# Kernel optimization log

Measured on AMD Instinct MI355X. Metric: run time of the kernel, lower is better.

Reference implementation:

```python
import jax, jax.numpy as jnp
import numpy as np

NUM_CAPSULE = 16
DIM_CAPSULE = 32
ROUTINGS = 4
EPS = 1e-07


def squash(x, axis=-1):
    # NOTE: faithful to the source: x / sqrt(sum(x^2) + eps) (unit-norm style),
    # NOT the standard Hinton squash.
    s2 = jnp.sum(x * x, axis=axis, keepdims=True)
    return x / jnp.sqrt(s2 + EPS)


def setup_inputs() -> dict:
    key = jax.random.key(0)
    k1, k2 = jax.random.split(key)
    B, N_in, D_in = 128, 1024, 256
    x = jax.random.normal(k1, (B, N_in, D_in), dtype=jnp.float32)
    # xavier_normal over (1, D_in, NUM_CAPSULE*DIM_CAPSULE)
    fan_in, fan_out = D_in, NUM_CAPSULE * DIM_CAPSULE
    std = np.sqrt(2.0 / (fan_in + fan_out))
    W = jax.random.normal(k2, (1, D_in, NUM_CAPSULE * DIM_CAPSULE), dtype=jnp.float32) * std
    return {"x": x, "W": W}


def reference(x, W):
    B, N_in, _ = x.shape
    # u_hat: [B, N_in, num_cap*dim_cap] -> [B, num_cap, N_in, dim_cap]
    u_hat = jnp.matmul(x, W[0])
    u_hat = u_hat.reshape(B, N_in, NUM_CAPSULE, DIM_CAPSULE).transpose(0, 2, 1, 3)

    b = jnp.zeros((B, NUM_CAPSULE, N_in), dtype=u_hat.dtype)
    outputs = None
    for i in range(ROUTINGS):
        # torch permutes to softmax over the num_capsule axis; equivalent to axis=1 here
        c = jax.nn.softmax(b, axis=1)                      # [B, num_cap, N_in]
        outputs = squash(jnp.einsum('bij,bijk->bik', c, u_hat))  # [B, num_cap, dim_cap]
        if i < ROUTINGS - 1:
            b = jnp.einsum('bik,bijk->bij', outputs, u_hat)
    return outputs
```

## Files before the change

### kernel.cpp

```cpp
#include <hip/hip_runtime.h>
#include <hip/hip_bf16.h>

typedef unsigned int u32;
typedef float f32x4 __attribute__((ext_vector_type(4)));
typedef __bf16 bf16x8 __attribute__((ext_vector_type(8)));

#define BATCH 128
#define NIN   1024
#define DIN   256
#define NC    16
#define DC    32
#define NCOL  512

__device__ __forceinline__ float bflo(u32 v){ return __uint_as_float(v << 16); }
__device__ __forceinline__ float bfhi(u32 v){ return __uint_as_float(v & 0xffff0000u); }
__device__ __forceinline__ u32 bfround(u32 ua){ return (ua + 0x7fffu + ((ua >> 16) & 1u)) >> 16; }
__device__ __forceinline__ u32 pack2(float a, float b){
    return (bfround(__float_as_uint(a)) & 0xffffu) | (bfround(__float_as_uint(b)) << 16);
}
__device__ __forceinline__ bf16x8 ldfrag(const u32* p){
    return __builtin_bit_cast(bf16x8, *(const uint4*)p);
}

__global__ __launch_bounds__(256) void k_wconv(const float* __restrict__ W, uint4* __restrict__ Wt2){
    int id = blockIdx.x * 256 + threadIdx.x;
    int l = id & 63, ks = (id >> 6) & 7, ntile = id >> 9;
    int n = ntile * 16 + (l & 15);
    int w0 = ks * 16 + (l >> 4) * 4;
    u32 r[4];
    #pragma unroll
    for (int e = 0; e < 4; e++){
        int w = w0 + e;
        r[e] = pack2(W[(size_t)(2 * w) * NCOL + n], W[(size_t)(2 * w + 1) * NCOL + n]);
    }
    Wt2[id] = make_uint4(r[0], r[1], r[2], r[3]);
}

__global__ __launch_bounds__(512) void k_gemm(const float* __restrict__ x, const uint4* __restrict__ Wt2,
                                              u32* __restrict__ uhat, float* __restrict__ y0){
    __shared__ __align__(16) u32 xl[64 * 128];
    const int t = threadIdx.x, jb = blockIdx.x, b = blockIdx.y;
    const int lane = t & 63, wv = t >> 6;
    const int l15 = lane & 15, q = lane >> 4;

    {
        const float4* xg = (const float4*)(x + ((size_t)b * NIN + jb * 64) * DIN);
        #pragma unroll
        for (int m = 0; m < 4; m++){
            int p = t + 512 * m;
            float4 a = xg[2 * p], c = xg[2 * p + 1];
            int j = p >> 5, wq = 4 * (p & 31);
            uint4 v;
            v.x = pack2(a.x, a.y); v.y = pack2(a.z, a.w);
            v.z = pack2(c.x, c.y); v.w = pack2(c.z, c.w);
            *(uint4*)&xl[j * 128 + ((wq + 4 * j) & 127)] = v;
        }
    }
    __syncthreads();

    f32x4 acc[4][4];
    #pragma unroll
    for (int mt = 0; mt < 4; mt++)
        #pragma unroll
        for (int nt = 0; nt < 4; nt++) acc[mt][nt] = (f32x4){0.f, 0.f, 0.f, 0.f};
    #pragma unroll
    for (int ks = 0; ks < 8; ks++){
        bf16x8 af[4], bfr[4];
        #pragma unroll
        for (int mt = 0; mt < 4; mt++){
            int jr = mt * 16 + l15;
            af[mt] = ldfrag(&xl[jr * 128 + ((ks * 16 + q * 4 + 4 * jr) & 127)]);
        }
        #pragma unroll
        for (int nt = 0; nt < 4; nt++)
            bfr[nt] = __builtin_bit_cast(bf16x8, Wt2[(size_t)(((wv * 4 + nt) * 8 + ks) * 64) + lane]);
        #pragma unroll
        for (int mt = 0; mt < 4; mt++)
            #pragma unroll
            for (int nt = 0; nt < 4; nt++)
                acc[mt][nt] = __builtin_amdgcn_mfma_f32_16x16x32_bf16(af[mt], bfr[nt], acc[mt][nt], 0, 0, 0);
    }

    #pragma unroll
    for (int nt = 0; nt < 4; nt++){
        float v = 0.f;
        #pragma unroll
        for (int mt = 0; mt < 4; mt++)
            #pragma unroll
            for (int r = 0; r < 4; r++) v += acc[mt][nt][r];
        v += __shfl_xor(v, 16);
        v += __shfl_xor(v, 32);
        if (lane < 16) atomicAdd(&y0[b * NCOL + wv * 64 + nt * 16 + lane], v);
    }

    u32* ub = uhat + (((size_t)b * NC + jb) * NCOL) * 32;
    #pragma unroll
    for (int nt = 0; nt < 4; nt++){
        int n = wv * 64 + nt * 16 + l15;
        #pragma unroll
        for (int mt = 0; mt < 4; mt++){
            uint2 v;
            v.x = pack2(acc[mt][nt][0], acc[mt][nt][1]);
            v.y = pack2(acc[mt][nt][2], acc[mt][nt][3]);
            *(uint2*)&ub[n * 32 + mt * 8 + q * 2] = v;
        }
    }
}

__device__ __forceinline__ int rot8(int n){ return (n + (n >> 3)) & 7; }

__global__ __launch_bounds__(256) void k_route_u(const u32* __restrict__ uhat, const float* __restrict__ o,
                                                 float* __restrict__ y){
    __shared__ __align__(16) u32 ul[NCOL * 32];
    __shared__ float ol[NCOL];
    __shared__ float bbc[NC * 68];
    const int jc = blockIdx.x, b = blockIdx.y, t = threadIdx.x;

    ol[t] = o[b * NCOL + t];
    ol[t + 256] = o[b * NCOL + t + 256];
    {
        const uint4* ug = (const uint4*)(uhat + ((size_t)(b * NC + jc)) * NCOL * 32);
        #pragma unroll
        for (int m = 0; m < 16; m++){
            int id = t + 256 * m;
            int n = id >> 3, jq = id & 7;
            ((uint4*)ul)[n * 8 + ((jq + rot8(n)) & 7)] = ug[id];
        }
    }
    __syncthreads();

    {
        int i = t >> 4, jq2 = t & 15;
        float o_[32];
        #pragma unroll
        for (int e = 0; e < 8; e++) *(float4*)&o_[4 * e] = *(const float4*)&ol[i * DC + 4 * e];
        float a0 = 0.f, a1 = 0.f, a2 = 0.f, a3 = 0.f;
        #pragma unroll
        for (int k = 0; k < 32; k++){
            int n = i * DC + k;
            uint2 v = *(const uint2*)&ul[n * 32 + ((2 * jq2 + 4 * rot8(n)) & 31)];
            float ok = o_[k];
            a0 += ok * bflo(v.x); a1 += ok * bfhi(v.x);
            a2 += ok * bflo(v.y); a3 += ok * bfhi(v.y);
        }
        *(float4*)&bbc[i * 68 + 4 * jq2] = make_float4(a0, a1, a2, a3);
    }
    __syncthreads();

    if (t < 64){
        float m = -1e30f;
        #pragma unroll
        for (int i = 0; i < NC; i++) m = fmaxf(m, bbc[i * 68 + t]);
        float s = 0.f;
        #pragma unroll
        for (int i = 0; i < NC; i++){ float e = __expf(bbc[i * 68 + t] - m); bbc[i * 68 + t] = e; s += e; }
        float inv = 1.f / s;
        #pragma unroll
        for (int i = 0; i < NC; i++) bbc[i * 68 + t] *= inv;
    }
    __syncthreads();

    #pragma unroll
    for (int h = 0; h < 2; h++){
        int n = t + 256 * h;
        int i = n >> 5;
        float s = 0.f;
        #pragma unroll
        for (int w4 = 0; w4 < 8; w4++){
            uint4 v = *(const uint4*)&ul[n * 32 + ((4 * w4 + 4 * rot8(n)) & 31)];
            float4 c0 = *(const float4*)&bbc[i * 68 + 8 * w4];
            float4 c1 = *(const float4*)&bbc[i * 68 + 8 * w4 + 4];
            s += c0.x * bflo(v.x) + c0.y * bfhi(v.x) + c0.z * bflo(v.y) + c0.w * bfhi(v.y)
               + c1.x * bflo(v.z) + c1.y * bfhi(v.z) + c1.z * bflo(v.w) + c1.w * bfhi(v.w);
        }
        atomicAdd(&y[b * NCOL + n], s);
    }
}

__global__ __launch_bounds__(512) void k_squash(const float* __restrict__ y, float* __restrict__ o,
                                                float* __restrict__ out, int final){
    int b = blockIdx.x, t = threadIdx.x;
    float v = y[b * NCOL + t];
    float s = v * v;
    s += __shfl_xor(s, 1); s += __shfl_xor(s, 2); s += __shfl_xor(s, 4);
    s += __shfl_xor(s, 8); s += __shfl_xor(s, 16);
    float r = v / sqrtf(s + 1e-7f);
    if (final) out[b * NCOL + t] = r;
    else       o[b * NCOL + t] = r;
}

extern "C" void kernel_launch(void* const* d_in, const int* in_sizes, int n_in,
                              void* d_out, int out_size, void* d_ws, size_t ws_size,
                              hipStream_t stream){
    const float* x = (const float*)d_in[0];
    const float* W = (const float*)d_in[1];
    float* out = (float*)d_out;
    float* f = (float*)d_ws;
    float* y    = f;
    float* o    = f + 65536;
    uint4* Wt2  = (uint4*)(f + 131072);
    u32*   uhat = (u32*)(f + 196608);

    hipMemsetAsync(y, 0, NCOL * BATCH * sizeof(float), stream);
    k_wconv<<<64, 256, 0, stream>>>(W, Wt2);
    k_gemm<<<dim3(16, BATCH), 512, 0, stream>>>(x, Wt2, uhat, y);
    k_squash<<<BATCH, 512, 0, stream>>>(y, o, out, 0);
    for (int it = 1; it < 4; it++){
        hipMemsetAsync(y, 0, NCOL * BATCH * sizeof(float), stream);
        k_route_u<<<dim3(16, BATCH), 256, 0, stream>>>(uhat, o, y);
        k_squash<<<BATCH, 512, 0, stream>>>(y, o, out, it == 3 ? 1 : 0);
    }
}
```

Baseline: 321.6 us.

## Replace atomics with partial-sum buffers, halve route chunk size, prefetch W fragments

The float atomicAdd reductions into y, and the memsets before them, are replaced by per-chunk partial-sum buffers. A combined reduce-plus-squash kernel sums those partials. The uhat layout is re-chunked into 32-column pieces so each routing block uses half the LDS (32KB) and the routing grid doubles to 32x128 blocks, aiming for higher occupancy. The GEMM also software-prefetches the next k-step's W fragments into registers. The cost is extra global traffic for the partial buffers and more registers held in the GEMM.

```diff
diff --git a/kernel.cpp b/kernel.cpp
--- a/kernel.cpp
+++ b/kernel.cpp
@@ -21,6 +21,7 @@
 __device__ __forceinline__ bf16x8 ldfrag(const u32* p){
     return __builtin_bit_cast(bf16x8, *(const uint4*)p);
 }
+__device__ __forceinline__ int rot4(int n){ return (n + (n >> 3) + (n >> 5)) & 3; }
 
 __global__ __launch_bounds__(256) void k_wconv(const float* __restrict__ W, uint4* __restrict__ Wt2){
     int id = blockIdx.x * 256 + threadIdx.x;
@@ -37,11 +38,16 @@
 }
 
 __global__ __launch_bounds__(512) void k_gemm(const float* __restrict__ x, const uint4* __restrict__ Wt2,
-                                              u32* __restrict__ uhat, float* __restrict__ y0){
+                                              u32* __restrict__ uhat, float* __restrict__ yp0){
     __shared__ __align__(16) u32 xl[64 * 128];
     const int t = threadIdx.x, jb = blockIdx.x, b = blockIdx.y;
     const int lane = t & 63, wv = t >> 6;
     const int l15 = lane & 15, q = lane >> 4;
+
+    uint4 bnx[4], bc[4];
+    #pragma unroll
+    for (int nt = 0; nt < 4; nt++)
+        bnx[nt] = Wt2[(size_t)(((wv * 4 + nt) * 8 + 0) * 64) + lane];
 
     {
         const float4* xg = (const float4*)(x + ((size_t)b * NIN + jb * 64) * DIN);
@@ -65,20 +71,24 @@
         for (int nt = 0; nt < 4; nt++) acc[mt][nt] = (f32x4){0.f, 0.f, 0.f, 0.f};
     #pragma unroll
     for (int ks = 0; ks < 8; ks++){
-        bf16x8 af[4], bfr[4];
+        bf16x8 af[4];
         #pragma unroll
         for (int mt = 0; mt < 4; mt++){
             int jr = mt * 16 + l15;
             af[mt] = ldfrag(&xl[jr * 128 + ((ks * 16 + q * 4 + 4 * jr) & 127)]);
         }
         #pragma unroll
-        for (int nt = 0; nt < 4; nt++)
-            bfr[nt] = __builtin_bit_cast(bf16x8, Wt2[(size_t)(((wv * 4 + nt) * 8 + ks) * 64) + lane]);
+        for (int nt = 0; nt < 4; nt++) bc[nt] = bnx[nt];
+        if (ks < 7){
+            #pragma unroll
+            for (int nt = 0; nt < 4; nt++)
+                bnx[nt] = Wt2[(size_t)(((wv * 4 + nt) * 8 + ks + 1) * 64) + lane];
+        }
         #pragma unroll
         for (int mt = 0; mt < 4; mt++)
             #pragma unroll
             for (int nt = 0; nt < 4; nt++)
-                acc[mt][nt] = __builtin_amdgcn_mfma_f32_16x16x32_bf16(af[mt], bfr[nt], acc[mt][nt], 0, 0, 0);
+                acc[mt][nt] = __builtin_amdgcn_mfma_f32_16x16x32_bf16(af[mt], __builtin_bit_cast(bf16x8, bc[nt]), acc[mt][nt], 0, 0, 0);
     }
 
     #pragma unroll
@@ -90,73 +100,76 @@
             for (int r = 0; r < 4; r++) v += acc[mt][nt][r];
         v += __shfl_xor(v, 16);
         v += __shfl_xor(v, 32);
-        if (lane < 16) atomicAdd(&y0[b * NCOL + wv * 64 + nt * 16 + lane], v);
-    }
-
-    u32* ub = uhat + (((size_t)b * NC + jb) * NCOL) * 32;
+        if (lane < 16)
+            yp0[((size_t)jb * BATCH + b) * NCOL + wv * 64 + nt * 16 + lane] = v;
+    }
+
+    u32* ub = uhat + (size_t)b * 32 * NCOL * 16;
     #pragma unroll
     for (int nt = 0; nt < 4; nt++){
         int n = wv * 64 + nt * 16 + l15;
         #pragma unroll
         for (int mt = 0; mt < 4; mt++){
+            int jp = mt * 8 + q * 2;
+            int ch = jb * 2 + (jp >> 4);
+            int wp = jp & 15;
             uint2 v;
             v.x = pack2(acc[mt][nt][0], acc[mt][nt][1]);
             v.y = pack2(acc[mt][nt][2], acc[mt][nt][3]);
-            *(uint2*)&ub[n * 32 + mt * 8 + q * 2] = v;
-        }
-    }
-}
-
-__device__ __forceinline__ int rot8(int n){ return (n + (n >> 3)) & 7; }
-
-__global__ __launch_bounds__(256) void k_route_u(const u32* __restrict__ uhat, const float* __restrict__ o,
-                                                 float* __restrict__ y){
-    __shared__ __align__(16) u32 ul[NCOL * 32];
+            *(uint2*)&ub[((size_t)ch * NCOL + n) * 16 + wp] = v;
+        }
+    }
+}
+
+__global__ __launch_bounds__(256) void k_route(const u32* __restrict__ uhat, const float* __restrict__ og,
+                                               float* __restrict__ yp){
+    __shared__ __align__(16) u32 ul[NCOL * 16];
     __shared__ float ol[NCOL];
-    __shared__ float bbc[NC * 68];
-    const int jc = blockIdx.x, b = blockIdx.y, t = threadIdx.x;
-
-    ol[t] = o[b * NCOL + t];
-    ol[t + 256] = o[b * NCOL + t + 256];
+    __shared__ float bbc[NC * 33];
+    const int ch = blockIdx.x, b = blockIdx.y, t = threadIdx.x;
+
+    ol[t] = og[b * NCOL + t];
+    ol[t + 256] = og[b * NCOL + t + 256];
     {
-        const uint4* ug = (const uint4*)(uhat + ((size_t)(b * NC + jc)) * NCOL * 32);
-        #pragma unroll
-        for (int m = 0; m < 16; m++){
+        const uint4* ug = (const uint4*)(uhat + ((size_t)b * 32 + ch) * NCOL * 16);
+        uint4* ul4 = (uint4*)ul;
+        #pragma unroll
+        for (int m = 0; m < 8; m++){
             int id = t + 256 * m;
-            int n = id >> 3, jq = id & 7;
-            ((uint4*)ul)[n * 8 + ((jq + rot8(n)) & 7)] = ug[id];
+            int n = id >> 2, s = id & 3;
+            ul4[n * 4 + ((s + rot4(n)) & 3)] = ug[id];
         }
     }
     __syncthreads();
 
     {
-        int i = t >> 4, jq2 = t & 15;
-        float o_[32];
-        #pragma unroll
-        for (int e = 0; e < 8; e++) *(float4*)&o_[4 * e] = *(const float4*)&ol[i * DC + 4 * e];
-        float a0 = 0.f, a1 = 0.f, a2 = 0.f, a3 = 0.f;
-        #pragma unroll
-        for (int k = 0; k < 32; k++){
+        int i = t >> 4, jq = t & 15;
+        float oc[DC];
+        #pragma unroll
+        for (int e = 0; e < 8; e++) *(float4*)&oc[4 * e] = *(const float4*)&ol[i * DC + 4 * e];
+        float a0 = 0.f, a1 = 0.f;
+        #pragma unroll
+        for (int k = 0; k < DC; k++){
             int n = i * DC + k;
-            uint2 v = *(const uint2*)&ul[n * 32 + ((2 * jq2 + 4 * rot8(n)) & 31)];
-            float ok = o_[k];
-            a0 += ok * bflo(v.x); a1 += ok * bfhi(v.x);
-            a2 += ok * bflo(v.y); a3 += ok * bfhi(v.y);
-        }
-        *(float4*)&bbc[i * 68 + 4 * jq2] = make_float4(a0, a1, a2, a3);
-    }
-    __syncthreads();
-
-    if (t < 64){
+            u32 v = ul[n * 16 + ((jq + 4 * rot4(n)) & 15)];
+            a0 += oc[k] * bflo(v);
+            a1 += oc[k] * bfhi(v);
+        }
+        bbc[i * 33 + 2 * jq]     = a0;
+        bbc[i * 33 + 2 * jq + 1] = a1;
+    }
+    __syncthreads();
+
+    if (t < 32){
         float m = -1e30f;
         #pragma unroll
-        for (int i = 0; i < NC; i++) m = fmaxf(m, bbc[i * 68 + t]);
+        for (int i = 0; i < NC; i++) m = fmaxf(m, bbc[i * 33 + t]);
         float s = 0.f;
         #pragma unroll
-        for (int i = 0; i < NC; i++){ float e = __expf(bbc[i * 68 + t] - m); bbc[i * 68 + t] = e; s += e; }
+        for (int i = 0; i < NC; i++){ float e = __expf(bbc[i * 33 + t] - m); bbc[i * 33 + t] = e; s += e; }
         float inv = 1.f / s;
         #pragma unroll
-        for (int i = 0; i < NC; i++) bbc[i * 68 + t] *= inv;
+        for (int i = 0; i < NC; i++) bbc[i * 33 + t] *= inv;
     }
     __syncthreads();
 
@@ -164,29 +177,35 @@
     for (int h = 0; h < 2; h++){
         int n = t + 256 * h;
         int i = n >> 5;
+        float cc[32];
+        #pragma unroll
+        for (int j = 0; j < 32; j++) cc[j] = bbc[i * 33 + j];
         float s = 0.f;
-        #pragma unroll
-        for (int w4 = 0; w4 < 8; w4++){
-            uint4 v = *(const uint4*)&ul[n * 32 + ((4 * w4 + 4 * rot8(n)) & 31)];
-            float4 c0 = *(const float4*)&bbc[i * 68 + 8 * w4];
-            float4 c1 = *(const float4*)&bbc[i * 68 + 8 * w4 + 4];
-            s += c0.x * bflo(v.x) + c0.y * bfhi(v.x) + c0.z * bflo(v.y) + c0.w * bfhi(v.y)
-               + c1.x * bflo(v.z) + c1.y * bfhi(v.z) + c1.z * bflo(v.w) + c1.w * bfhi(v.w);
-        }
-        atomicAdd(&y[b * NCOL + n], s);
-    }
-}
-
-__global__ __launch_bounds__(512) void k_squash(const float* __restrict__ y, float* __restrict__ o,
-                                                float* __restrict__ out, int final){
-    int b = blockIdx.x, t = threadIdx.x;
-    float v = y[b * NCOL + t];
-    float s = v * v;
-    s += __shfl_xor(s, 1); s += __shfl_xor(s, 2); s += __shfl_xor(s, 4);
-    s += __shfl_xor(s, 8); s += __shfl_xor(s, 16);
-    float r = v / sqrtf(s + 1e-7f);
-    if (final) out[b * NCOL + t] = r;
-    else       o[b * NCOL + t] = r;
+        const uint4* ul4 = (const uint4*)ul;
+        #pragma unroll
+        for (int s4 = 0; s4 < 4; s4++){
+            uint4 v = ul4[n * 4 + ((s4 + rot4(n)) & 3)];
+            int j0 = s4 * 8;
+            s += cc[j0+0] * bflo(v.x) + cc[j0+1] * bfhi(v.x)
+               + cc[j0+2] * bflo(v.y) + cc[j0+3] * bfhi(v.y)
+               + cc[j0+4] * bflo(v.z) + cc[j0+5] * bfhi(v.z)
+               + cc[j0+6] * bflo(v.w) + cc[j0+7] * bfhi(v.w);
+        }
+        yp[((size_t)ch * BATCH + b) * NCOL + n] = s;
+    }
+}
+
+__global__ __launch_bounds__(512) void k_sz(const float* __restrict__ yp, int P,
+                                            float* __restrict__ og, float* __restrict__ out, int final){
+    const int b = blockIdx.x, t = threadIdx.x;
+    float s = 0.f;
+    for (int p = 0; p < P; p++) s += yp[((size_t)p * BATCH + b) * NCOL + t];
+    float v = s * s;
+    v += __shfl_xor(v, 1); v += __shfl_xor(v, 2); v += __shfl_xor(v, 4);
+    v += __shfl_xor(v, 8); v += __shfl_xor(v, 16);
+    float o = s / sqrtf(v + 1e-7f);
+    og[b * NCOL + t] = o;
+    if (final) out[(size_t)b * NCOL + t] = o;
 }
 
 extern "C" void kernel_launch(void* const* d_in, const int* in_sizes, int n_in,
@@ -196,18 +215,17 @@
     const float* W = (const float*)d_in[1];
     float* out = (float*)d_out;
     float* f = (float*)d_ws;
-    float* y    = f;
-    float* o    = f + 65536;
-    uint4* Wt2  = (uint4*)(f + 131072);
-    u32*   uhat = (u32*)(f + 196608);
-
-    hipMemsetAsync(y, 0, NCOL * BATCH * sizeof(float), stream);
+    float* og   = f;
+    float* yp0  = f + 65536;
+    float* ypr  = f + 65536 + 1048576;
+    uint4* Wt2  = (uint4*)(f + 65536 + 1048576 + 2097152);
+    u32*   uhat = (u32*)(f + 65536 + 1048576 + 2097152 + 65536);
+
     k_wconv<<<64, 256, 0, stream>>>(W, Wt2);
-    k_gemm<<<dim3(16, BATCH), 512, 0, stream>>>(x, Wt2, uhat, y);
-    k_squash<<<BATCH, 512, 0, stream>>>(y, o, out, 0);
+    k_gemm<<<dim3(16, BATCH), 512, 0, stream>>>(x, Wt2, uhat, yp0);
+    k_sz<<<BATCH, 512, 0, stream>>>(yp0, 16, og, out, 0);
     for (int it = 1; it < 4; it++){
-        hipMemsetAsync(y, 0, NCOL * BATCH * sizeof(float), stream);
-        k_route_u<<<dim3(16, BATCH), 256, 0, stream>>>(uhat, o, y);
-        k_squash<<<BATCH, 512, 0, stream>>>(y, o, out, it == 3 ? 1 : 0);
-    }
-}
+        k_route<<<dim3(32, BATCH), 256, 0, stream>>>(uhat, og, ypr);
+        k_sz<<<BATCH, 512, 0, stream>>>(ypr, 32, og, out, it == 3 ? 1 : 0);
+    }
+}
```

Measured after the change: 340.8 us. 6.0% more time.
